# Kernel tuning notes

Hardware: AMD Instinct MI355X
Metric: run time of the kernel (lower is better)

## Reference

```python
import jax, jax.numpy as jnp
import numpy as np

D = 1024        # embedding_dim
H = 16          # num_heads
HKV = 4         # num_kv_heads
HD = D // H     # head_dim = 64
L = 64          # latent_dim
EPS = 1e-6
LN_EPS = 1e-5
B, S = 2, 1024


def _feat(x):
    # feature_map == 'elu': elu(x) + 1 (non-negative features)
    return jax.nn.elu(x) + 1.0


def setup_inputs() -> dict:
    key = jax.random.key(0)
    ks = jax.random.split(key, 8)
    w = lambda k, shape: (jax.random.normal(k, shape, jnp.float32) * 0.02)
    return {
        "x": jax.random.normal(ks[0], (B, S, D), jnp.float32),
        "Wq": w(ks[1], (D, D)), "bq": jnp.zeros((D,), jnp.float32),
        "Wk": w(ks[2], (D, HKV * HD)), "bk": jnp.zeros((HKV * HD,), jnp.float32),
        "Wv": w(ks[3], (D, HKV * HD)), "bv": jnp.zeros((HKV * HD,), jnp.float32),
        "Wc": w(ks[4], (HKV * HD, L)),   # kv_compress (no bias)
        "We": w(ks[5], (L, HKV * HD)),   # kv_expand (no bias)
        "Wo": w(ks[6], (D, D)), "bo": jnp.zeros((D,), jnp.float32),
        "gamma": jnp.ones((D,), jnp.float32),
        "beta": jnp.zeros((D,), jnp.float32),
    }


def reference(x, Wq, bq, Wk, bk, Wv, bv, Wc, We, Wo, bo, gamma, beta):
    b, s, _ = x.shape
    residual = x
    # projections
    q = x @ Wq + bq                     # [b,s,D]
    k = x @ Wk + bk                     # [b,s,HKV*HD]
    v = x @ Wv + bv
    # latent compress -> expand
    k = (k @ Wc) @ We                   # [b,s,HKV*HD]
    v = (v @ Wc) @ We
    # split heads
    q = q.reshape(b, s, H, HD).transpose(0, 2, 1, 3)      # [b,H,s,HD]
    k = k.reshape(b, s, HKV, HD).transpose(0, 2, 1, 3)    # [b,HKV,s,HD]
    v = v.reshape(b, s, HKV, HD).transpose(0, 2, 1, 3)
    # GQA: repeat KV heads per query group
    rep = H // HKV
    k = jnp.repeat(k, rep, axis=1)                        # [b,H,s,HD]
    v = jnp.repeat(v, rep, axis=1)
    # causal linear attention via cumulative KV outer-product state
    qf = _feat(q)                                          # [b,h,s,f]
    kf = _feat(k)
    kv = jnp.einsum('bhsf,bhsd->bhsfd', kf, v)             # [b,h,s,f,d]
    kv_cum = jnp.cumsum(kv, axis=2)
    num = jnp.einsum('bhsf,bhsfd->bhsd', qf, kv_cum)
    den = jnp.einsum('bhsf,bhsf->bhs', qf, jnp.cumsum(kf, axis=2))[..., None] + EPS
    o = num / den                                          # [b,h,s,d]
    # merge heads, output projection
    o = o.transpose(0, 2, 1, 3).reshape(b, s, D)
    o = o @ Wo + bo
    # residual + layernorm (epsilon=1e-5)
    y = residual + o
    mu = jnp.mean(y, axis=-1, keepdims=True)
    var = jnp.var(y, axis=-1, keepdims=True)
    return (y - mu) / jnp.sqrt(var + LN_EPS) * gamma + beta
```

## Files before the change

### kernel.cpp

```cpp
#include <hip/hip_runtime.h>

#define D_ 1024
#define H_ 16
#define HKV_ 4
#define B_ 2
#define S_ 1024
#define BS_ (B_*S_)
#define QKVW 1536
#define QB 64
#define NC (S_/QB)

typedef short bf8 __attribute__((ext_vector_type(8)));
typedef float f32x4 __attribute__((ext_vector_type(4)));

#define MFMA_B16(a,b,c) __builtin_amdgcn_mfma_f32_16x16x32_bf16((a),(b),(c),0,0,0)

#define GLOAD16(g, l) __builtin_amdgcn_global_load_lds( \
    (const __attribute__((address_space(1))) void*)(g), \
    (__attribute__((address_space(3))) void*)(l), 16, 0, 0)

#define SW(row, idx) ((idx) ^ (((row) & 7) << 3))

__device__ __forceinline__ unsigned short f2b(float f) {
  unsigned int u = __float_as_uint(f);
  u += 0x7FFFu + ((u >> 16) & 1u);
  return (unsigned short)(u >> 16);
}
__device__ __forceinline__ float b2f(unsigned short h) {
  return __uint_as_float(((unsigned int)h) << 16);
}
__device__ __forceinline__ float feat(float x) { return x > 0.f ? x + 1.f : __expf(x); }

__device__ __forceinline__ void conv_body(const float* __restrict__ src,
                                          unsigned short* __restrict__ dst,
                                          int sub, int n4, int tid) {
  int i = sub * 256 + tid;
  if (i >= n4) return;
  float4 v = ((const float4*)src)[i];
  ushort4 o;
  o.x = f2b(v.x); o.y = f2b(v.y); o.z = f2b(v.z); o.w = f2b(v.w);
  ((ushort4*)dst)[i] = o;
}

__device__ __forceinline__ void tconv_body(const float* __restrict__ src,
                                           unsigned short* __restrict__ dst,
                                           int bx, int by, int ss, int ds,
                                           int tid, float (*tl)[65]) {
  int r0 = by * 64, c0 = bx * 64;
  int ty = tid >> 4, tx4 = (tid & 15) * 4;
#pragma unroll
  for (int rep = 0; rep < 4; ++rep) {
    int r = ty + rep * 16;
    float4 v = *(const float4*)&src[(size_t)(r0 + r) * ss + c0 + tx4];
    tl[r][tx4] = v.x; tl[r][tx4 + 1] = v.y; tl[r][tx4 + 2] = v.z; tl[r][tx4 + 3] = v.w;
  }
  __syncthreads();
#pragma unroll
  for (int rep = 0; rep < 4; ++rep) {
    int c = ty + rep * 16;
    ushort4 o;
    o.x = f2b(tl[tx4 + 0][c]); o.y = f2b(tl[tx4 + 1][c]);
    o.z = f2b(tl[tx4 + 2][c]); o.w = f2b(tl[tx4 + 3][c]);
    *(ushort4*)&dst[(size_t)(c0 + c) * ds + r0 + tx4] = o;
  }
}

__global__ __launch_bounds__(256) void k_prep(const float* __restrict__ x,
                                              const float* __restrict__ Wq,
                                              const float* __restrict__ Wo,
                                              const float* __restrict__ Wk,
                                              const float* __restrict__ Wv,
                                              const float* __restrict__ Wc,
                                              const float* __restrict__ We,
                                              unsigned short* __restrict__ xb,
                                              unsigned short* __restrict__ Wqkv_t,
                                              unsigned short* __restrict__ Wo_t,
                                              unsigned short* __restrict__ Wkv_b,
                                              float* __restrict__ Wce,
                                              unsigned short* __restrict__ Wce_t) {
  __shared__ float tl[64][65];
  __shared__ __align__(16) unsigned short As[64][72];
  __shared__ __align__(16) unsigned short Bs[128][72];
  int blk = blockIdx.x, tid = threadIdx.x;
  if (blk < 2048) {
    conv_body(x, xb, blk, BS_ * D_ / 4, tid);
  } else if (blk < 2304) {
    conv_body(Wk, Wkv_b, blk - 2048, 1024 * 256 / 4, tid);
  } else if (blk < 2560) {
    conv_body(Wv, Wkv_b + 1024 * 256, blk - 2304, 1024 * 256 / 4, tid);
  } else if (blk < 2816) {
    int sb = blk - 2560;
    tconv_body(Wq, Wqkv_t, sb & 15, sb >> 4, 1024, 1024, tid, tl);
  } else if (blk < 3072) {
    int sb = blk - 2816;
    tconv_body(Wo, Wo_t, sb & 15, sb >> 4, 1024, 1024, tid, tl);
  } else {
    int sb = blk - 3072;
    int row0 = (sb >> 1) * 64, col0 = (sb & 1) * 128;
    {
      int r = tid >> 2, c0 = (tid & 3) * 16;
      const float* src = &Wc[(size_t)(row0 + r) * 64 + c0];
#pragma unroll
      for (int e = 0; e < 16; e += 4) {
        float4 v = *(const float4*)(src + e);
        As[r][c0 + e] = f2b(v.x); As[r][c0 + e + 1] = f2b(v.y);
        As[r][c0 + e + 2] = f2b(v.z); As[r][c0 + e + 3] = f2b(v.w);
      }
      int k = tid >> 2, cb = (tid & 3) * 32;
      const float* wsrc = &We[(size_t)k * 256 + col0 + cb];
#pragma unroll
      for (int e = 0; e < 32; e += 4) {
        float4 v = *(const float4*)(wsrc + e);
        Bs[cb + e][k] = f2b(v.x); Bs[cb + e + 1][k] = f2b(v.y);
        Bs[cb + e + 2][k] = f2b(v.z); Bs[cb + e + 3][k] = f2b(v.w);
      }
    }
    __syncthreads();
    const int lane = tid & 63, wave = tid >> 6;
    const int lr = lane & 15, lq = lane >> 4;
    const int wc0 = wave * 32;
    const f32x4 fzero = {0.f, 0.f, 0.f, 0.f};
    f32x4 acc[4][2];
#pragma unroll
    for (int i = 0; i < 4; ++i) { acc[i][0] = fzero; acc[i][1] = fzero; }
#pragma unroll
    for (int kk = 0; kk < 2; ++kk)
#pragma unroll
      for (int mi = 0; mi < 4; ++mi) {
        bf8 a = *(const bf8*)&As[mi * 16 + lr][kk * 32 + lq * 8];
#pragma unroll
        for (int ni = 0; ni < 2; ++ni) {
          bf8 bb = *(const bf8*)&Bs[wc0 + ni * 16 + lr][kk * 32 + lq * 8];
          acc[mi][ni] = MFMA_B16(a, bb, acc[mi][ni]);
        }
      }
#pragma unroll
    for (int mi = 0; mi < 4; ++mi)
#pragma unroll
      for (int ni = 0; ni < 2; ++ni) {
        int col = col0 + wc0 + ni * 16 + lr;
#pragma unroll
        for (int r = 0; r < 4; ++r) {
          int row = row0 + mi * 16 + lq * 4 + r;
          float v = acc[mi][ni][r];
          Wce[(size_t)row * 256 + col] = v;
          Wce_t[(size_t)col * 256 + row] = f2b(v);
        }
      }
  }
}

template<int MODE>
__global__ __launch_bounds__(64) void k_gemm1(const unsigned short* __restrict__ A,
                                              const unsigned short* __restrict__ Bt,
                                              const float* __restrict__ bias,
                                              unsigned short* __restrict__ C,
                                              int N, int K) {
  __shared__ __align__(16) unsigned short As[2][64 * 64];
  __shared__ __align__(16) unsigned short Bs[2][64 * 64];
  const int lane = threadIdx.x;
  const int row0 = blockIdx.y * 64, col0 = blockIdx.x * 64;
  const int lr = lane & 15, lq = lane >> 4;
  const int rsub = lane >> 3, sj = lane & 7;
  const int js = sj ^ rsub;
  const f32x4 fzero = {0.f, 0.f, 0.f, 0.f};
  f32x4 acc[4][4];
#pragma unroll
  for (int i = 0; i < 4; ++i)
#pragma unroll
    for (int j = 0; j < 4; ++j) acc[i][j] = fzero;

#define STAGE64(pb, k0)                                                        \
  {                                                                            \
    _Pragma("unroll")                                                          \
    for (int i = 0; i < 8; ++i)                                                \
      GLOAD16(&A[(size_t)(row0 + i * 8 + rsub) * K + (k0) + js * 8],           \
              &As[pb][(i * 512 + lane * 8)]);                                  \
    _Pragma("unroll")                                                          \
    for (int i = 0; i < 8; ++i)                                                \
      GLOAD16(&Bt[(size_t)(col0 + i * 8 + rsub) * K + (k0) + js * 8],          \
              &Bs[pb][(i * 512 + lane * 8)]);                                  \
  }

  STAGE64(0, 0);
  int cur = 0;
  for (int k0 = 0; k0 < K; k0 += 64) {
    if (k0 + 64 < K) {
      STAGE64(cur ^ 1, k0 + 64);
      asm volatile("s_waitcnt vmcnt(16)" ::: "memory");
    } else {
      asm volatile("s_waitcnt vmcnt(0)" ::: "memory");
    }
    __builtin_amdgcn_sched_barrier(0);
    bf8 af[2][4], bfr[2][4];
#pragma unroll
    for (int kk = 0; kk < 2; ++kk)
#pragma unroll
      for (int mi = 0; mi < 4; ++mi) {
        int ch = (kk * 4 + lq) ^ (lr & 7);
        af[kk][mi]  = *(const bf8*)&As[cur][(mi * 16 + lr) * 64 + ch * 8];
        bfr[kk][mi] = *(const bf8*)&Bs[cur][(mi * 16 + lr) * 64 + ch * 8];
      }
#pragma unroll
    for (int kk = 0; kk < 2; ++kk)
#pragma unroll
      for (int mi = 0; mi < 4; ++mi)
#pragma unroll
        for (int ni = 0; ni < 4; ++ni)
          acc[mi][ni] = MFMA_B16(af[kk][mi], bfr[kk][ni], acc[mi][ni]);
    cur ^= 1;
  }
#undef STAGE64
#pragma unroll
  for (int ni = 0; ni < 4; ++ni) {
    int col = col0 + ni * 16 + lr;
    float bv = bias[col];
#pragma unroll
    for (int mi = 0; mi < 4; ++mi)
#pragma unroll
      for (int r = 0; r < 4; ++r) {
        int row = row0 + mi * 16 + lq * 4 + r;
        float v = acc[mi][ni][r] + bv;
        if (MODE == 1 && col < 1280) v = feat(v);
        C[(size_t)row * N + col] = f2b(v);
      }
  }
}

__global__ __launch_bounds__(128) void k_fold(const unsigned short* __restrict__ A,
                                              const unsigned short* __restrict__ Bt,
                                              unsigned short* __restrict__ C,
                                              float* __restrict__ biasq,
                                              int N, int K,
                                              const float* __restrict__ fbq,
                                              const float* __restrict__ fbk,
                                              const float* __restrict__ fbv,
                                              const float* __restrict__ fWce) {
  if (blockIdx.y == 4) {
    int t = blockIdx.x * 128 + threadIdx.x;
    if (t >= QKVW) return;
    if (t < 1024) { biasq[t] = fbq[t]; return; }
    const float* b = (t < 1280) ? fbk : fbv;
    int n = (t < 1280) ? (t - 1024) : (t - 1280);
    float s = 0.f;
    for (int j = 0; j < 256; ++j) s += b[j] * fWce[j * 256 + n];
    biasq[t] = s;
    return;
  }
  __shared__ __align__(16) unsigned short As[64 * 32];
  __shared__ __align__(16) unsigned short Bs[128 * 32];
  const int tid = threadIdx.x;
  const int lane = tid & 63, wave = tid >> 6;
  const int row0 = blockIdx.y * 64, col0 = blockIdx.x * 128;
  const f32x4 fzero = {0.f, 0.f, 0.f, 0.f};
  f32x4 acc[4][4];
#pragma unroll
  for (int i = 0; i < 4; ++i)
#pragma unroll
    for (int j = 0; j < 4; ++j) acc[i][j] = fzero;
  const int lr = lane & 15, lq = lane >> 4, lk = lq * 8;
  for (int k0 = 0; k0 < K; k0 += 32) {
#pragma unroll
    for (int i = 0; i < 2; ++i) {
      int e = (tid + i * 128) * 8;
      int r = e >> 5, c = e & 31;
      GLOAD16(&A[(size_t)(row0 + r) * K + k0 + c], &As[e]);
    }
#pragma unroll
    for (int i = 0; i < 4; ++i) {
      int e = (tid + i * 128) * 8;
      int r = e >> 5, c = e & 31;
      GLOAD16(&Bt[(size_t)(col0 + r) * K + k0 + c], &Bs[e]);
    }
    __syncthreads();
    bf8 af[4], bfr[4];
#pragma unroll
    for (int mi = 0; mi < 4; ++mi)
      af[mi] = *(const bf8*)&As[(mi * 16 + lr) * 32 + lk];
#pragma unroll
    for (int ni = 0; ni < 4; ++ni)
      bfr[ni] = *(const bf8*)&Bs[(wave * 64 + ni * 16 + lr) * 32 + lk];
#pragma unroll
    for (int mi = 0; mi < 4; ++mi)
#pragma unroll
      for (int ni = 0; ni < 4; ++ni)
        acc[mi][ni] = MFMA_B16(af[mi], bfr[ni], acc[mi][ni]);
    __syncthreads();
  }
#pragma unroll
  for (int mi = 0; mi < 4; ++mi)
#pragma unroll
    for (int ni = 0; ni < 4; ++ni) {
      int col = col0 + wave * 64 + ni * 16 + lr;
#pragma unroll
      for (int r = 0; r < 4; ++r) {
        int row = row0 + mi * 16 + lq * 4 + r;
        int sec = col >> 10, cc = col & 1023;
        C[(size_t)(1024 + sec * 256 + row) * 1024 + cc] = f2b(acc[mi][ni][r]);
      }
    }
}

__global__ __launch_bounds__(256) void k_vkv(const unsigned short* __restrict__ qkvb,
                                             float* __restrict__ stc) {
  __shared__ unsigned short tl[64][72];
  __shared__ float Kf[64 * 64];
  int c = blockIdx.x, g = blockIdx.y, b = blockIdx.z;
  int tid = threadIdx.x;
  int s0 = c * QB;
  {
    int j = tid >> 2, f0 = (tid & 3) * 16;
    const unsigned short* kr = &qkvb[(size_t)(b * S_ + s0 + j) * QKVW + 1024 + g * 64 + f0];
    const unsigned short* vr = &qkvb[(size_t)(b * S_ + s0 + j) * QKVW + 1280 + g * 64 + f0];
    uint4 k0_ = *(const uint4*)kr;
    uint4 k1_ = *(const uint4*)(kr + 8);
    const unsigned short* ks = (const unsigned short*)&k0_;
#pragma unroll
    for (int e = 0; e < 8; ++e) Kf[j * 64 + f0 + e] = b2f(ks[e]);
    ks = (const unsigned short*)&k1_;
#pragma unroll
    for (int e = 0; e < 8; ++e) Kf[j * 64 + f0 + 8 + e] = b2f(ks[e]);
    *(uint4*)&tl[j][f0] = *(const uint4*)vr;
    *(uint4*)&tl[j][f0 + 8] = *(const uint4*)(vr + 8);
  }
  __syncthreads();
  int d = tid >> 2, f0 = (tid & 3) * 16;
  float acc[16];
#pragma unroll
  for (int e = 0; e < 16; ++e) acc[e] = 0.f;
#pragma unroll 4
  for (int j = 0; j < QB; ++j) {
    float vv = b2f(tl[j][d]);
    const float* kfr = &Kf[j * 64 + f0];
#pragma unroll
    for (int e = 0; e < 16; ++e) acc[e] += vv * kfr[e];
  }
  size_t base = ((size_t)((b * HKV_ + g) * NC + c) * 65 + d) * 64 + f0;
#pragma unroll
  for (int e = 0; e < 16; ++e) stc[base + e] = acc[e];
  if (tid < 64) {
    float z = 0.f;
    for (int j = 0; j < QB; ++j) z += Kf[j * 64 + tid];
    stc[((size_t)((b * HKV_ + g) * NC + c) * 65 + 64) * 64 + tid] = z;
  }
}

__global__ __launch_bounds__(512) void k_attn(const unsigned short* __restrict__ qkvb,
                                              const float* __restrict__ stc,
                                              unsigned short* __restrict__ ob) {
  __shared__ __align__(16) unsigned short Kf[64 * 64];
  __shared__ __align__(16) unsigned short Vl[64 * 64];
  __shared__ __align__(16) unsigned short Sl[64 * 64];
  __shared__ __align__(16) unsigned short P[2][64 * 64];
  __shared__ float zl[64];
  __shared__ float qz[2][64];
  __shared__ float den[2][64];
  int c = blockIdx.x, hp = blockIdx.y, b = blockIdx.z;
  int g = hp >> 1;
  int tid = threadIdx.x, lane = tid & 63, wave = tid >> 6;
  int s0 = c * QB;
  const int lr = lane & 15, lq = lane >> 4, lk = lq * 8;
  const int hh = wave >> 2, rw = (wave & 3) * 16;
  unsigned short* Pv = &P[0][0];

  {
    int t = tid & 255;
    int j = t >> 2, f0 = (t & 3) * 16;
    if (tid < 256) {
      const unsigned short* kr =
          &qkvb[(size_t)(b * S_ + s0 + j) * QKVW + 1024 + g * 64 + f0];
      *(uint4*)&Kf[SW(j, j * 64 + f0)]     = *(const uint4*)kr;
      *(uint4*)&Kf[SW(j, j * 64 + f0 + 8)] = *(const uint4*)(kr + 8);
    } else {
      const unsigned short* vr =
          &qkvb[(size_t)(b * S_ + s0 + j) * QKVW + 1280 + g * 64 + f0];
      *(uint4*)&Pv[j * 72 + f0]     = *(const uint4*)vr;
      *(uint4*)&Pv[j * 72 + f0 + 8] = *(const uint4*)(vr + 8);
    }
  }
  {
    int dd = tid >> 3, col = (tid & 7) * 8;
    const float* sb = stc + (size_t)(b * HKV_ + g) * NC * 4160 + dd * 64 + col;
    float p0[8], p1[8], p2[8], p3[8];
#pragma unroll
    for (int e = 0; e < 8; ++e) { p0[e] = 0.f; p1[e] = 0.f; p2[e] = 0.f; p3[e] = 0.f; }
    int cc = 0;
    for (; cc + 4 <= c; cc += 4) {
      const float* q0 = sb + (size_t)(cc + 0) * 4160;
      const float* q1 = sb + (size_t)(cc + 1) * 4160;
      const float* q2 = sb + (size_t)(cc + 2) * 4160;
      const float* q3 = sb + (size_t)(cc + 3) * 4160;
      float4 a0 = *(const float4*)q0, b0 = *(const float4*)(q0 + 4);
      float4 a1 = *(const float4*)q1, b1 = *(const float4*)(q1 + 4);
      float4 a2 = *(const float4*)q2, b2 = *(const float4*)(q2 + 4);
      float4 a3 = *(const float4*)q3, b3 = *(const float4*)(q3 + 4);
      p0[0] += a0.x; p0[1] += a0.y; p0[2] += a0.z; p0[3] += a0.w;
      p0[4] += b0.x; p0[5] += b0.y; p0[6] += b0.z; p0[7] += b0.w;
      p1[0] += a1.x; p1[1] += a1.y; p1[2] += a1.z; p1[3] += a1.w;
      p1[4] += b1.x; p1[5] += b1.y; p1[6] += b1.z; p1[7] += b1.w;
      p2[0] += a2.x; p2[1] += a2.y; p2[2] += a2.z; p2[3] += a2.w;
      p2[4] += b2.x; p2[5] += b2.y; p2[6] += b2.z; p2[7] += b2.w;
      p3[0] += a3.x; p3[1] += a3.y; p3[2] += a3.z; p3[3] += a3.w;
      p3[4] += b3.x; p3[5] += b3.y; p3[6] += b3.z; p3[7] += b3.w;
    }
    for (; cc < c; ++cc) {
      const float* q0 = sb + (size_t)cc * 4160;
      float4 a0 = *(const float4*)q0, b0 = *(const float4*)(q0 + 4);
      p0[0] += a0.x; p0[1] += a0.y; p0[2] += a0.z; p0[3] += a0.w;
      p0[4] += b0.x; p0[5] += b0.y; p0[6] += b0.z; p0[7] += b0.w;
    }
    unsigned short o[8];
#pragma unroll
    for (int e = 0; e < 8; ++e) o[e] = f2b(p0[e] + p1[e] + p2[e] + p3[e]);
    *(uint4*)&Sl[SW(dd, dd * 64 + col)] = *(const uint4*)o;
    if (tid < 64) {
      const float* zb = stc + (size_t)(b * HKV_ + g) * NC * 4160 + 64 * 64 + tid;
      float z0 = 0.f, z1 = 0.f, z2 = 0.f, z3 = 0.f;
      int c2 = 0;
      for (; c2 + 4 <= c; c2 += 4) {
        z0 += zb[(size_t)(c2 + 0) * 4160];
        z1 += zb[(size_t)(c2 + 1) * 4160];
        z2 += zb[(size_t)(c2 + 2) * 4160];
        z3 += zb[(size_t)(c2 + 3) * 4160];
      }
      for (; c2 < c; ++c2) z0 += zb[(size_t)c2 * 4160];
      zl[tid] = z0 + z1 + z2 + z3;
    }
  }
  bf8 aQ[2];
  {
    const unsigned short* qr =
        &qkvb[(size_t)(b * S_ + s0 + rw + lr) * QKVW + (hp * 2 + hh) * 64];
    aQ[0] = *(const bf8*)(qr + lk);
    aQ[1] = *(const bf8*)(qr + 32 + lk);
  }
  __syncthreads();
  {
    int d = tid >> 3, sq = (tid & 7) * 8;
    unsigned short tmp[8];
#pragma unroll
    for (int e = 0; e < 8; ++e) tmp[e] = Pv[(sq + e) * 72 + d];
    *(uint4*)&Vl[SW(d, d * 64 + sq)] = *(const uint4*)tmp;
  }
  {
    float qdot = 0.f;
#pragma unroll
    for (int kk = 0; kk < 2; ++kk)
#pragma unroll
      for (int e = 0; e < 8; ++e)
        qdot += b2f((unsigned short)aQ[kk][e]) * zl[kk * 32 + lq * 8 + e];
    qdot += __shfl_xor(qdot, 16);
    qdot += __shfl_xor(qdot, 32);
    if (lq == 0) qz[hh][rw + lr] = qdot;
  }
  __syncthreads();
  const f32x4 fzero = {0.f, 0.f, 0.f, 0.f};
  f32x4 sc[4];
#pragma unroll
  for (int nj = 0; nj < 4; ++nj) sc[nj] = fzero;
#pragma unroll
  for (int nj = 0; nj < 4; ++nj)
#pragma unroll
    for (int kk = 0; kk < 2; ++kk) {
      bf8 bk8 = *(const bf8*)&Kf[SW(nj * 16 + lr, (nj * 16 + lr) * 64 + kk * 32 + lk)];
      sc[nj] = MFMA_B16(aQ[kk], bk8, sc[nj]);
    }
#pragma unroll
  for (int nj = 0; nj < 4; ++nj)
#pragma unroll
    for (int r = 0; r < 4; ++r) {
      int i = rw + lq * 4 + r;
      int j = nj * 16 + lr;
      float v = (j <= i) ? sc[nj][r] : 0.f;
      P[hh][SW(i, i * 64 + j)] = f2b(v);
    }
  __syncthreads();
  {
    int hd = tid >> 8, t = tid & 255;
    int i = t >> 2, q = t & 3, f0 = q * 16;
    float s = 0.f;
#pragma unroll
    for (int e = 0; e < 16; ++e) s += b2f(P[hd][SW(i, i * 64 + f0 + e)]);
    s += __shfl_xor(s, 1);
    s += __shfl_xor(s, 2);
    if (q == 0) den[hd][i] = s + qz[hd][i];
  }
  f32x4 oa[4];
#pragma unroll
  for (int nd = 0; nd < 4; ++nd) oa[nd] = fzero;
  bf8 aP[2];
#pragma unroll
  for (int kk = 0; kk < 2; ++kk)
    aP[kk] = *(const bf8*)&P[hh][SW(rw + lr, (rw + lr) * 64 + kk * 32 + lk)];
#pragma unroll
  for (int nd = 0; nd < 4; ++nd)
#pragma unroll
    for (int kk = 0; kk < 2; ++kk) {
      bf8 bS = *(const bf8*)&Sl[SW(nd * 16 + lr, (nd * 16 + lr) * 64 + kk * 32 + lk)];
      oa[nd] = MFMA_B16(aQ[kk], bS, oa[nd]);
      bf8 bV = *(const bf8*)&Vl[SW(nd * 16 + lr, (nd * 16 + lr) * 64 + kk * 32 + lk)];
      oa[nd] = MFMA_B16(aP[kk], bV, oa[nd]);
    }
  __syncthreads();
#pragma unroll
  for (int nd = 0; nd < 4; ++nd)
#pragma unroll
    for (int r = 0; r < 4; ++r) {
      int i = rw + lq * 4 + r;
      int dd = nd * 16 + lr;
      P[0][0] = P[0][0];
      (&P[0][0])[i * 128 + hh * 64 + dd] = f2b(oa[nd][r] / (den[hh][i] + 1e-6f));
    }
  __syncthreads();
  {
    int j = tid >> 3, u = tid & 7;
    unsigned short* orow = &ob[(size_t)(b * S_ + s0 + j) * D_ + hp * 128 + u * 16];
    *(uint4*)orow       = *(const uint4*)&(&P[0][0])[j * 128 + u * 16];
    *(uint4*)(orow + 8) = *(const uint4*)&(&P[0][0])[j * 128 + u * 16 + 8];
  }
}

__global__ __launch_bounds__(256) void k_ln(const unsigned short* __restrict__ xb,
                                            const unsigned short* __restrict__ o2,
                                            const float* __restrict__ gamma,
                                            const float* __restrict__ beta,
                                            float* __restrict__ out) {
  int row = blockIdx.x, tid = threadIdx.x;
  ushort4 xv = ((const ushort4*)(xb + (size_t)row * D_))[tid];
  ushort4 ov = ((const ushort4*)(o2 + (size_t)row * D_))[tid];
  float4 y;
  y.x = b2f(xv.x) + b2f(ov.x); y.y = b2f(xv.y) + b2f(ov.y);
  y.z = b2f(xv.z) + b2f(ov.z); y.w = b2f(xv.w) + b2f(ov.w);
  float s = y.x + y.y + y.z + y.w;
  float ss = y.x * y.x + y.y * y.y + y.z * y.z + y.w * y.w;
#pragma unroll
  for (int off = 32; off > 0; off >>= 1) {
    s += __shfl_down(s, off);
    ss += __shfl_down(ss, off);
  }
  __shared__ float red[8];
  int lane = tid & 63, wave = tid >> 6;
  if (lane == 0) { red[wave] = s; red[4 + wave] = ss; }
  __syncthreads();
  if (tid == 0) {
    red[0] = red[0] + red[1] + red[2] + red[3];
    red[4] = red[4] + red[5] + red[6] + red[7];
  }
  __syncthreads();
  float mu = red[0] * (1.f / D_);
  float var = red[4] * (1.f / D_) - mu * mu;
  float rs = rsqrtf(var + 1e-5f);
  float4 g4 = ((const float4*)gamma)[tid];
  float4 b4 = ((const float4*)beta)[tid];
  float4 o;
  o.x = (y.x - mu) * rs * g4.x + b4.x;
  o.y = (y.y - mu) * rs * g4.y + b4.y;
  o.z = (y.z - mu) * rs * g4.z + b4.z;
  o.w = (y.w - mu) * rs * g4.w + b4.w;
  ((float4*)(out + (size_t)row * D_))[tid] = o;
}

extern "C" void kernel_launch(void* const* d_in, const int* in_sizes, int n_in,
                              void* d_out, int out_size, void* d_ws, size_t ws_size,
                              hipStream_t stream) {
  const float* x     = (const float*)d_in[0];
  const float* Wq    = (const float*)d_in[1];
  const float* bq    = (const float*)d_in[2];
  const float* Wk    = (const float*)d_in[3];
  const float* bk    = (const float*)d_in[4];
  const float* Wv    = (const float*)d_in[5];
  const float* bv    = (const float*)d_in[6];
  const float* Wc    = (const float*)d_in[7];
  const float* We    = (const float*)d_in[8];
  const float* Wo    = (const float*)d_in[9];
  const float* bo    = (const float*)d_in[10];
  const float* gamma = (const float*)d_in[11];
  const float* beta  = (const float*)d_in[12];

  char* p = (char*)d_ws;
  size_t off = 0;
  auto carve = [&](size_t bytes) {
    void* r = p + off;
    off = (off + bytes + 255) & ~(size_t)255;
    return r;
  };
  unsigned short* xb     = (unsigned short*)carve((size_t)BS_ * D_ * 2);
  unsigned short* Wqkv_t = (unsigned short*)carve((size_t)QKVW * D_ * 2);
  unsigned short* Wo_t   = (unsigned short*)carve((size_t)D_ * D_ * 2);
  float*          biasq  = (float*)carve(QKVW * 4);
  unsigned short* qkvb   = (unsigned short*)carve((size_t)BS_ * QKVW * 2);
  float*          Wce    = (float*)carve(256 * 256 * 4);
  unsigned short* Wce_t  = (unsigned short*)carve(256 * 256 * 2);
  unsigned short* Wkv_b  = (unsigned short*)carve((size_t)2048 * 256 * 2);
  float*          stc    = (float*)carve((size_t)8 * NC * 65 * 64 * 4);
  unsigned short* obuf   = (unsigned short*)carve((size_t)BS_ * D_ * 2);
  unsigned short* o2     = (unsigned short*)carve((size_t)BS_ * D_ * 2);

  k_prep<<<3080, 256, 0, stream>>>(x, Wq, Wo, Wk, Wv, Wc, We,
                                   xb, Wqkv_t, Wo_t, Wkv_b, Wce, Wce_t);
  k_fold<<<dim3(16, 5), 128, 0, stream>>>(Wce_t, Wkv_b, Wqkv_t, biasq,
                                          2048, 256, bq, bk, bv, Wce);
  k_gemm1<1><<<dim3(24, 32), 64, 0, stream>>>(xb, Wqkv_t, biasq, qkvb, QKVW, 1024);
  k_vkv<<<dim3(NC, HKV_, B_), 256, 0, stream>>>(qkvb, stc);
  k_attn<<<dim3(NC, H_ / 2, B_), 512, 0, stream>>>(qkvb, stc, obuf);
  k_gemm1<0><<<dim3(16, 32), 64, 0, stream>>>(obuf, Wo_t, bo, o2, 1024, 1024);
  k_ln<<<BS_, 256, 0, stream>>>(xb, o2, gamma, beta, (float*)d_out);
}
```

Measured before the change: 87.19 us.

## Fold Wc·We weight composition and bias fold into prep kernel, drop k_fold

Moves the folded K/V weight computation (Wk·Wc·We, Wv·Wc·We) and the folded bias into extra blocks of k_prep, computing Wc·We per block in LDS then multiplying by fp32 Wk/Wv converted on the fly. This removes the separate k_fold launch and the intermediate Wkv_b/Wce/Wce_t buffers and their global round trips. The trade is that each of the 64 fold blocks recomputes a slice of the Wc·We product and does an unpipelined K loop, which could lengthen the prep kernel's tail.

New measurement: 81.44 us, median of 2. -6.6%, faster.

```diff
diff --git a/kernel.cpp b/kernel.cpp
--- a/kernel.cpp
+++ b/kernel.cpp
@@ -72,81 +72,144 @@
                                               const float* __restrict__ Wv,
                                               const float* __restrict__ Wc,
                                               const float* __restrict__ We,
+                                              const float* __restrict__ bq,
+                                              const float* __restrict__ bk,
+                                              const float* __restrict__ bv,
                                               unsigned short* __restrict__ xb,
                                               unsigned short* __restrict__ Wqkv_t,
                                               unsigned short* __restrict__ Wo_t,
-                                              unsigned short* __restrict__ Wkv_b,
-                                              float* __restrict__ Wce,
-                                              unsigned short* __restrict__ Wce_t) {
-  __shared__ float tl[64][65];
-  __shared__ __align__(16) unsigned short As[64][72];
-  __shared__ __align__(16) unsigned short Bs[128][72];
+                                              float* __restrict__ biasq) {
+  __shared__ __align__(16) unsigned char smem[46080];
   int blk = blockIdx.x, tid = threadIdx.x;
   if (blk < 2048) {
     conv_body(x, xb, blk, BS_ * D_ / 4, tid);
   } else if (blk < 2304) {
-    conv_body(Wk, Wkv_b, blk - 2048, 1024 * 256 / 4, tid);
+    int sb = blk - 2048;
+    tconv_body(Wq, Wqkv_t, sb & 15, sb >> 4, 1024, 1024, tid, (float(*)[65])smem);
   } else if (blk < 2560) {
-    conv_body(Wv, Wkv_b + 1024 * 256, blk - 2304, 1024 * 256 / 4, tid);
-  } else if (blk < 2816) {
+    int sb = blk - 2304;
+    tconv_body(Wo, Wo_t, sb & 15, sb >> 4, 1024, 1024, tid, (float(*)[65])smem);
+  } else if (blk < 2624) {
     int sb = blk - 2560;
-    tconv_body(Wq, Wqkv_t, sb & 15, sb >> 4, 1024, 1024, tid, tl);
-  } else if (blk < 3072) {
-    int sb = blk - 2816;
-    tconv_body(Wo, Wo_t, sb & 15, sb >> 4, 1024, 1024, tid, tl);
-  } else {
-    int sb = blk - 3072;
-    int row0 = (sb >> 1) * 64, col0 = (sb & 1) * 128;
+    int bx = sb & 15, by = sb >> 4;
+    int col0 = bx * 128, row0 = by * 64;
+    unsigned short (*Aw)[72] = (unsigned short(*)[72])smem;
+    unsigned short (*Bc)[72] = (unsigned short(*)[72])(smem + 64 * 72 * 2);
     {
-      int r = tid >> 2, c0 = (tid & 3) * 16;
-      const float* src = &Wc[(size_t)(row0 + r) * 64 + c0];
+      int j = tid >> 2, c4 = (tid & 3) * 16;
+      const float* src = &We[(size_t)j * 256 + row0 + c4];
 #pragma unroll
       for (int e = 0; e < 16; e += 4) {
         float4 v = *(const float4*)(src + e);
-        As[r][c0 + e] = f2b(v.x); As[r][c0 + e + 1] = f2b(v.y);
-        As[r][c0 + e + 2] = f2b(v.z); As[r][c0 + e + 3] = f2b(v.w);
-      }
-      int k = tid >> 2, cb = (tid & 3) * 32;
-      const float* wsrc = &We[(size_t)k * 256 + col0 + cb];
-#pragma unroll
-      for (int e = 0; e < 32; e += 4) {
+        Aw[c4 + e + 0][j] = f2b(v.x); Aw[c4 + e + 1][j] = f2b(v.y);
+        Aw[c4 + e + 2][j] = f2b(v.z); Aw[c4 + e + 3][j] = f2b(v.w);
+      }
+      const float* wsrc = &Wc[(size_t)tid * 64];
+#pragma unroll
+      for (int e = 0; e < 64; e += 4) {
         float4 v = *(const float4*)(wsrc + e);
-        Bs[cb + e][k] = f2b(v.x); Bs[cb + e + 1][k] = f2b(v.y);
-        Bs[cb + e + 2][k] = f2b(v.z); Bs[cb + e + 3][k] = f2b(v.w);
+        Bc[tid][e + 0] = f2b(v.x); Bc[tid][e + 1] = f2b(v.y);
+        Bc[tid][e + 2] = f2b(v.z); Bc[tid][e + 3] = f2b(v.w);
       }
     }
     __syncthreads();
     const int lane = tid & 63, wave = tid >> 6;
     const int lr = lane & 15, lq = lane >> 4;
-    const int wc0 = wave * 32;
     const f32x4 fzero = {0.f, 0.f, 0.f, 0.f};
-    f32x4 acc[4][2];
-#pragma unroll
-    for (int i = 0; i < 4; ++i) { acc[i][0] = fzero; acc[i][1] = fzero; }
+    f32x4 tacc[4][4];
+#pragma unroll
+    for (int i = 0; i < 4; ++i)
+#pragma unroll
+      for (int j = 0; j < 4; ++j) tacc[i][j] = fzero;
 #pragma unroll
     for (int kk = 0; kk < 2; ++kk)
 #pragma unroll
       for (int mi = 0; mi < 4; ++mi) {
-        bf8 a = *(const bf8*)&As[mi * 16 + lr][kk * 32 + lq * 8];
+        bf8 a = *(const bf8*)&Aw[mi * 16 + lr][kk * 32 + lq * 8];
+#pragma unroll
+        for (int ni = 0; ni < 4; ++ni) {
+          bf8 bb = *(const bf8*)&Bc[wave * 64 + ni * 16 + lr][kk * 32 + lq * 8];
+          tacc[mi][ni] = MFMA_B16(a, bb, tacc[mi][ni]);
+        }
+      }
+    __syncthreads();
+    unsigned short (*T)[264] = (unsigned short(*)[264])smem;
+#pragma unroll
+    for (int mi = 0; mi < 4; ++mi)
+#pragma unroll
+      for (int ni = 0; ni < 4; ++ni) {
+        int k = wave * 64 + ni * 16 + lr;
+#pragma unroll
+        for (int r = 0; r < 4; ++r)
+          T[mi * 16 + lq * 4 + r][k] = f2b(tacc[mi][ni][r]);
+      }
+    __syncthreads();
+    unsigned short (*Bs)[40] = (unsigned short(*)[40])(smem + 64 * 264 * 2);
+    f32x4 acc2[4][2];
+#pragma unroll
+    for (int i = 0; i < 4; ++i) { acc2[i][0] = fzero; acc2[i][1] = fzero; }
+    for (int k0 = 0; k0 < 256; k0 += 32) {
+      {
+        int colr = tid >> 1, half = tid & 1;
+        int col = col0 + colr;
+        const float* src = (col < 1024)
+            ? &Wk[(size_t)col * 256 + k0 + half * 16]
+            : &Wv[(size_t)(col - 1024) * 256 + k0 + half * 16];
+#pragma unroll
+        for (int e = 0; e < 16; e += 4) {
+          float4 v = *(const float4*)(src + e);
+          Bs[colr][half * 16 + e + 0] = f2b(v.x);
+          Bs[colr][half * 16 + e + 1] = f2b(v.y);
+          Bs[colr][half * 16 + e + 2] = f2b(v.z);
+          Bs[colr][half * 16 + e + 3] = f2b(v.w);
+        }
+      }
+      __syncthreads();
+#pragma unroll
+      for (int mi = 0; mi < 4; ++mi) {
+        bf8 a = *(const bf8*)&T[mi * 16 + lr][k0 + lq * 8];
 #pragma unroll
         for (int ni = 0; ni < 2; ++ni) {
-          bf8 bb = *(const bf8*)&Bs[wc0 + ni * 16 + lr][kk * 32 + lq * 8];
-          acc[mi][ni] = MFMA_B16(a, bb, acc[mi][ni]);
+          bf8 bb = *(const bf8*)&Bs[wave * 32 + ni * 16 + lr][lq * 8];
+          acc2[mi][ni] = MFMA_B16(a, bb, acc2[mi][ni]);
         }
       }
+      __syncthreads();
+    }
 #pragma unroll
     for (int mi = 0; mi < 4; ++mi)
 #pragma unroll
       for (int ni = 0; ni < 2; ++ni) {
-        int col = col0 + wc0 + ni * 16 + lr;
+        int col = col0 + wave * 32 + ni * 16 + lr;
+        int sec = col >> 10, cc = col & 1023;
 #pragma unroll
         for (int r = 0; r < 4; ++r) {
           int row = row0 + mi * 16 + lq * 4 + r;
-          float v = acc[mi][ni][r];
-          Wce[(size_t)row * 256 + col] = v;
-          Wce_t[(size_t)col * 256 + row] = f2b(v);
+          Wqkv_t[(size_t)(1024 + sec * 256 + row) * 1024 + cc] = f2b(acc2[mi][ni][r]);
         }
       }
+  } else if (blk == 2624) {
+    float* tb = (float*)smem;
+    if (tid < 128) {
+      int l = tid & 63;
+      const float* bsrc = (tid < 64) ? bk : bv;
+      float s = 0.f;
+      for (int j = 0; j < 256; ++j) s += bsrc[j] * Wc[(size_t)j * 64 + l];
+      tb[tid] = s;
+    }
+    __syncthreads();
+    {
+      float s0 = 0.f, s1 = 0.f;
+      for (int l = 0; l < 64; ++l) {
+        float w = We[(size_t)l * 256 + tid];
+        s0 += tb[l] * w;
+        s1 += tb[64 + l] * w;
+      }
+      biasq[1024 + tid] = s0;
+      biasq[1280 + tid] = s1;
+    }
+  } else {
+    ((float4*)biasq)[tid] = ((const float4*)bq)[tid];
   }
 }
 
@@ -225,80 +288,6 @@
         C[(size_t)row * N + col] = f2b(v);
       }
   }
-}
-
-__global__ __launch_bounds__(128) void k_fold(const unsigned short* __restrict__ A,
-                                              const unsigned short* __restrict__ Bt,
-                                              unsigned short* __restrict__ C,
-                                              float* __restrict__ biasq,
-                                              int N, int K,
-                                              const float* __restrict__ fbq,
-                                              const float* __restrict__ fbk,
-                                              const float* __restrict__ fbv,
-                                              const float* __restrict__ fWce) {
-  if (blockIdx.y == 4) {
-    int t = blockIdx.x * 128 + threadIdx.x;
-    if (t >= QKVW) return;
-    if (t < 1024) { biasq[t] = fbq[t]; return; }
-    const float* b = (t < 1280) ? fbk : fbv;
-    int n = (t < 1280) ? (t - 1024) : (t - 1280);
-    float s = 0.f;
-    for (int j = 0; j < 256; ++j) s += b[j] * fWce[j * 256 + n];
-    biasq[t] = s;
-    return;
-  }
-  __shared__ __align__(16) unsigned short As[64 * 32];
-  __shared__ __align__(16) unsigned short Bs[128 * 32];
-  const int tid = threadIdx.x;
-  const int lane = tid & 63, wave = tid >> 6;
-  const int row0 = blockIdx.y * 64, col0 = blockIdx.x * 128;
-  const f32x4 fzero = {0.f, 0.f, 0.f, 0.f};
-  f32x4 acc[4][4];
-#pragma unroll
-  for (int i = 0; i < 4; ++i)
-#pragma unroll
-    for (int j = 0; j < 4; ++j) acc[i][j] = fzero;
-  const int lr = lane & 15, lq = lane >> 4, lk = lq * 8;
-  for (int k0 = 0; k0 < K; k0 += 32) {
-#pragma unroll
-    for (int i = 0; i < 2; ++i) {
-      int e = (tid + i * 128) * 8;
-      int r = e >> 5, c = e & 31;
-      GLOAD16(&A[(size_t)(row0 + r) * K + k0 + c], &As[e]);
-    }
-#pragma unroll
-    for (int i = 0; i < 4; ++i) {
-      int e = (tid + i * 128) * 8;
-      int r = e >> 5, c = e & 31;
-      GLOAD16(&Bt[(size_t)(col0 + r) * K + k0 + c], &Bs[e]);
-    }
-    __syncthreads();
-    bf8 af[4], bfr[4];
-#pragma unroll
-    for (int mi = 0; mi < 4; ++mi)
-      af[mi] = *(const bf8*)&As[(mi * 16 + lr) * 32 + lk];
-#pragma unroll
-    for (int ni = 0; ni < 4; ++ni)
-      bfr[ni] = *(const bf8*)&Bs[(wave * 64 + ni * 16 + lr) * 32 + lk];
-#pragma unroll
-    for (int mi = 0; mi < 4; ++mi)
-#pragma unroll
-      for (int ni = 0; ni < 4; ++ni)
-        acc[mi][ni] = MFMA_B16(af[mi], bfr[ni], acc[mi][ni]);
-    __syncthreads();
-  }
-#pragma unroll
-  for (int mi = 0; mi < 4; ++mi)
-#pragma unroll
-    for (int ni = 0; ni < 4; ++ni) {
-      int col = col0 + wave * 64 + ni * 16 + lr;
-#pragma unroll
-      for (int r = 0; r < 4; ++r) {
-        int row = row0 + mi * 16 + lq * 4 + r;
-        int sec = col >> 10, cc = col & 1023;
-        C[(size_t)(1024 + sec * 256 + row) * 1024 + cc] = f2b(acc[mi][ni][r]);
-      }
-    }
 }
 
 __global__ __launch_bounds__(256) void k_vkv(const unsigned short* __restrict__ qkvb,
@@ -508,7 +497,6 @@
     for (int r = 0; r < 4; ++r) {
       int i = rw + lq * 4 + r;
       int dd = nd * 16 + lr;
-      P[0][0] = P[0][0];
       (&P[0][0])[i * 128 + hh * 64 + dd] = f2b(oa[nd][r] / (den[hh][i] + 1e-6f));
     }
   __syncthreads();
@@ -589,17 +577,12 @@
   unsigned short* Wo_t   = (unsigned short*)carve((size_t)D_ * D_ * 2);
   float*          biasq  = (float*)carve(QKVW * 4);
   unsigned short* qkvb   = (unsigned short*)carve((size_t)BS_ * QKVW * 2);
-  float*          Wce    = (float*)carve(256 * 256 * 4);
-  unsigned short* Wce_t  = (unsigned short*)carve(256 * 256 * 2);
-  unsigned short* Wkv_b  = (unsigned short*)carve((size_t)2048 * 256 * 2);
   float*          stc    = (float*)carve((size_t)8 * NC * 65 * 64 * 4);
   unsigned short* obuf   = (unsigned short*)carve((size_t)BS_ * D_ * 2);
   unsigned short* o2     = (unsigned short*)carve((size_t)BS_ * D_ * 2);
 
-  k_prep<<<3080, 256, 0, stream>>>(x, Wq, Wo, Wk, Wv, Wc, We,
-                                   xb, Wqkv_t, Wo_t, Wkv_b, Wce, Wce_t);
-  k_fold<<<dim3(16, 5), 128, 0, stream>>>(Wce_t, Wkv_b, Wqkv_t, biasq,
-                                          2048, 256, bq, bk, bv, Wce);
+  k_prep<<<2626, 256, 0, stream>>>(x, Wq, Wo, Wk, Wv, Wc, We, bq, bk, bv,
+                                   xb, Wqkv_t, Wo_t, biasq);
   k_gemm1<1><<<dim3(24, 32), 64, 0, stream>>>(xb, Wqkv_t, biasq, qkvb, QKVW, 1024);
   k_vkv<<<dim3(NC, HKV_, B_), 256, 0, stream>>>(qkvb, stc);
   k_attn<<<dim3(NC, H_ / 2, B_), 512, 0, stream>>>(qkvb, stc, obuf);
```
